# Kernel optimization log

Hardware: AMD Instinct MI355X
Metric: run time of the kernel (lower is better)

## Reference

```python
import jax, jax.numpy as jnp
import numpy as np
import math

B, S, D, H = 2, 2048, 512, 8
DK = D // H  # 64
NEG_INF = float('-inf')


def setup_inputs() -> dict:
    key = jax.random.key(0)
    ks = jax.random.split(key, 16)
    s = 1.0 / math.sqrt(D)
    return {
        'in_Q': jax.random.normal(ks[0], (B, S, D), jnp.float32),
        'in_K': jax.random.normal(ks[1], (B, S, D), jnp.float32),
        'in_V': jax.random.normal(ks[2], (B, S, D), jnp.float32),
        'row_pad_mask': jax.random.randint(ks[3], (B, S), 0, 2, jnp.int32),
        'col_pad_mask': jax.random.randint(ks[4], (B, S), 0, 2, jnp.int32),
        'W_Q': jax.random.uniform(ks[5], (D, D), jnp.float32, -s, s),
        'b_Q': jax.random.uniform(ks[6], (D,), jnp.float32, -s, s),
        'W_K': jax.random.uniform(ks[7], (D, D), jnp.float32, -s, s),
        'b_K': jax.random.uniform(ks[8], (D,), jnp.float32, -s, s),
        'W_V': jax.random.uniform(ks[9], (D, D), jnp.float32, -s, s),
        'b_V': jax.random.uniform(ks[10], (D,), jnp.float32, -s, s),
        'W_O': jax.random.uniform(ks[11], (D, D), jnp.float32, -s, s),
        'b_O': jax.random.uniform(ks[12], (D,), jnp.float32, -s, s),
    }


def reference(in_Q, in_K, in_V, row_pad_mask, col_pad_mask,
              W_Q, b_Q, W_K, b_K, W_V, b_V, W_O, b_O):
    b, sq, _ = in_Q.shape
    sk = in_K.shape[1]
    # projections (torch Linear: x @ W.T + b)
    Q = in_Q @ W_Q.T + b_Q
    K = in_K @ W_K.T + b_K
    V = in_V @ W_V.T + b_V
    # chunk along feature dim + stack == reshape to heads: [b, h, s, dk]
    Qh = Q.reshape(b, sq, H, DK).transpose(0, 2, 1, 3)
    Kh = K.reshape(b, sk, H, DK).transpose(0, 2, 1, 3)
    Vh = V.reshape(b, sk, H, DK).transpose(0, 2, 1, 3)
    scores = jnp.einsum('bhqd,bhkd->bhqk', Qh, Kh) / math.sqrt(DK)
    # causal mask (additive -inf above diagonal, as in the original)
    causal = jnp.triu(jnp.full((sq, sk), NEG_INF, scores.dtype), k=1)
    scores = scores + causal
    # padding masks: pad masks encode lengths via their row sums
    row_len = row_pad_mask.sum(axis=1)  # [b]
    col_len = col_pad_mask.sum(axis=1)
    row_np = jnp.arange(sq)[None, :] < row_len[:, None]  # [b, sq]
    col_np = jnp.arange(sk)[None, :] < col_len[:, None]  # [b, sk]
    non_pad = (row_np[:, :, None] & col_np[:, None, :])[:, None]  # [b,1,sq,sk]
    scores = jnp.where(non_pad, scores, NEG_INF)
    p = jax.nn.softmax(scores, axis=-1)
    p = jnp.nan_to_num(p)  # fully-masked rows -> 0 (matches torch nan_to_num)
    attn = jnp.einsum('bhqk,bhkd->bhqd', p, Vh)
    Hcat = attn.transpose(0, 2, 1, 3).reshape(b, sq, D)
    return Hcat @ W_O.T + b_O
```

## Files before the change

### kernel.cpp

```cpp
#include <hip/hip_runtime.h>

#define S_LEN 2048
#define D_MODEL 512
#define NHEAD 8
#define BATCH 2

typedef __attribute__((ext_vector_type(8))) short bf16x8;
typedef __attribute__((ext_vector_type(4))) float f32x4;

__device__ __forceinline__ unsigned short f2bf(float f) {
    union { float f; unsigned u; } v; v.f = f;
    unsigned u = v.u + 0x7FFFu + ((v.u >> 16) & 1u);
    return (unsigned short)(u >> 16);
}

__device__ __forceinline__ float ex2(float x) {
    return __builtin_amdgcn_exp2f(x);
}

__device__ __forceinline__ unsigned cvtpk(float lo, float hi) {
    unsigned r;
    asm("v_cvt_pk_bf16_f32 %0, %1, %2" : "=v"(r) : "v"(lo), "v"(hi));
    return r;
}

__device__ __forceinline__ void gl_lds16(const unsigned short* g, unsigned short* l) {
    __builtin_amdgcn_global_load_lds(
        (const __attribute__((address_space(1))) void*)g,
        (__attribute__((address_space(3))) void*)l,
        16, 0, 0);
}

__global__ __launch_bounds__(256) void cvtlens_kernel(
    const float* __restrict__ inQ, const float* __restrict__ inK, const float* __restrict__ inV,
    const float* __restrict__ WQ, const float* __restrict__ WK,
    const float* __restrict__ WV, const float* __restrict__ WO,
    const int* __restrict__ rpm, const int* __restrict__ cpm,
    unsigned short* __restrict__ Xbf, unsigned short* __restrict__ Wbf,
    int* __restrict__ lens)
{
    const int t = threadIdx.x;
    if (blockIdx.x < 2) {
        __shared__ int red[256];
        const int b = blockIdx.x;
        int sr = 0, sc2 = 0;
        for (int i = t; i < S_LEN; i += 256) {
            sr  += rpm[b * S_LEN + i];
            sc2 += cpm[b * S_LEN + i];
        }
        red[t] = sr;
        __syncthreads();
        for (int off = 128; off > 0; off >>= 1) {
            if (t < off) red[t] += red[t + off];
            __syncthreads();
        }
        if (t == 0) lens[b * 2 + 0] = red[0];
        __syncthreads();
        red[t] = sc2;
        __syncthreads();
        for (int off = 128; off > 0; off >>= 1) {
            if (t < off) red[t] += red[t + off];
            __syncthreads();
        }
        if (t == 0) lens[b * 2 + 1] = red[0];
    }

    const int NXC = 786432;
    const int NTOT = 917504;
    const int stride = gridDim.x * 256;
    for (int c = blockIdx.x * 256 + t; c < NTOT; c += stride) {
        if (c < NXC) {
            const int flat = c << 3;
            const int z = flat >> 21;
            const int off = flat & 2097151;
            const float* src = ((z == 0) ? inQ : (z == 1) ? inK : inV) + off;
            float4 a = *(const float4*)src;
            float4 d = *(const float4*)(src + 4);
            unsigned short* w = Xbf + flat;
            w[0] = f2bf(a.x); w[1] = f2bf(a.y); w[2] = f2bf(a.z); w[3] = f2bf(a.w);
            w[4] = f2bf(d.x); w[5] = f2bf(d.y); w[6] = f2bf(d.z); w[7] = f2bf(d.w);
        } else {
            const int wflat = (c - NXC) << 3;
            const int wz = wflat >> 18;
            const int off = wflat & 262143;
            const float* src = ((wz == 0) ? WQ : (wz == 1) ? WK : (wz == 2) ? WV : WO) + off;
            float4 a = *(const float4*)src;
            float4 d = *(const float4*)(src + 4);
            unsigned short* w = Wbf + wflat;
            w[0] = f2bf(a.x); w[1] = f2bf(a.y); w[2] = f2bf(a.z); w[3] = f2bf(a.w);
            w[4] = f2bf(d.x); w[5] = f2bf(d.y); w[6] = f2bf(d.z); w[7] = f2bf(d.w);
        }
    }
}

__global__ __launch_bounds__(256) void proj_gemm(
    const unsigned short* __restrict__ Xbf, const unsigned short* __restrict__ Wbf,
    const float* __restrict__ bQ, const float* __restrict__ bK, const float* __restrict__ bV,
    const int* __restrict__ lens,
    unsigned short* __restrict__ Qg, unsigned short* __restrict__ Kg,
    unsigned short* __restrict__ VTg)
{
    __shared__ __align__(16) unsigned short Xld[2][8192];
    __shared__ __align__(16) unsigned short Wld[2][8192];

    const int z = blockIdx.z;
    const int tileS = blockIdx.x * 128;
    const int tileF = blockIdx.y * 128;
    const int bb0 = tileS >> 11;
    const int rl = lens[bb0 * 2], cl = lens[bb0 * 2 + 1];
    const int limit = (z == 0) ? rl : cl;
    if ((tileS & 2047) >= limit) return;

    const unsigned short* X = Xbf + (size_t)z * (4096 * 512);
    const unsigned short* W = Wbf + (size_t)z * (512 * 512);
    const float* bias = (z == 0) ? bQ : (z == 1) ? bK : bV;

    const int t = threadIdx.x;
    const int wv = t >> 6, lane = t & 63, l15 = lane & 15, quad = lane >> 4;
    const int ro = lane >> 3;
    const int lc8 = ((lane & 7) ^ ro) * 8;

    const unsigned short* gX = X + (size_t)(tileS + wv * 32 + ro) * 512 + lc8;
    const unsigned short* gW = W + (size_t)(tileF + wv * 32 + ro) * 512 + lc8;
    const int wvo = wv * 2048;

    const int f_off = (wv & 1) * 64, s_off = (wv >> 1) * 64;
    const int swk = l15 & 7;

    f32x4 acc[4][4] = {};

    #pragma unroll
    for (int j = 0; j < 4; ++j) {
        gl_lds16(gX + j * 4096, &Xld[0][wvo + j * 512]);
        gl_lds16(gW + j * 4096, &Wld[0][wvo + j * 512]);
    }

    for (int kk = 0; kk < 8; ++kk) {
        __syncthreads();
        if (kk < 7) {
            const int k0 = (kk + 1) * 64;
            const int nb = (kk + 1) & 1;
            #pragma unroll
            for (int j = 0; j < 4; ++j) {
                gl_lds16(gX + k0 + j * 4096, &Xld[nb][wvo + j * 512]);
                gl_lds16(gW + k0 + j * 4096, &Wld[nb][wvo + j * 512]);
            }
        }
        const unsigned short* Xb = Xld[kk & 1];
        const unsigned short* Wb = Wld[kk & 1];
        #pragma unroll
        for (int kk2 = 0; kk2 < 2; ++kk2) {
            bf16x8 wf[4], xf[4];
            #pragma unroll
            for (int i = 0; i < 4; ++i) {
                const int rw = f_off + i * 16 + l15;
                wf[i] = *(const bf16x8*)(Wb + rw * 64 + ((kk2 * 4 + quad) ^ swk) * 8);
                const int rx = s_off + i * 16 + l15;
                xf[i] = *(const bf16x8*)(Xb + rx * 64 + ((kk2 * 4 + quad) ^ swk) * 8);
            }
            #pragma unroll
            for (int ft = 0; ft < 4; ++ft)
                #pragma unroll
                for (int st = 0; st < 4; ++st)
                    acc[ft][st] = __builtin_amdgcn_mfma_f32_16x16x32_bf16(
                        wf[ft], xf[st], acc[ft][st], 0, 0, 0);
        }
    }

    const float oscale = (z == 0) ? 0.18033688011112042f : 1.0f;
    #pragma unroll
    for (int ft = 0; ft < 4; ++ft) {
        const int f = tileF + f_off + ft * 16 + quad * 4;
        const int h = f >> 6, dk = f & 63;
        const float b0 = bias[f], b1 = bias[f + 1], b2 = bias[f + 2], b3 = bias[f + 3];
        #pragma unroll
        for (int st = 0; st < 4; ++st) {
            const int s = tileS + s_off + st * 16 + l15;
            const int bb = s >> 11, seq = s & 2047;
            const f32x4 a = acc[ft][st];
            if (z <= 1) {
                unsigned short* dst = ((z == 0) ? Qg : Kg)
                    + ((size_t)((bb * 8 + h) * 2048 + seq)) * 64 + dk;
                ushort4 u;
                u.x = f2bf((a[0] + b0) * oscale); u.y = f2bf((a[1] + b1) * oscale);
                u.z = f2bf((a[2] + b2) * oscale); u.w = f2bf((a[3] + b3) * oscale);
                *(ushort4*)dst = u;
            } else {
                unsigned short* dst = VTg
                    + ((size_t)((bb * 8 + h) * 64 + dk)) * 2048 + seq;
                dst[0]    = f2bf(a[0] + b0);
                dst[2048] = f2bf(a[1] + b1);
                dst[4096] = f2bf(a[2] + b2);
                dst[6144] = f2bf(a[3] + b3);
            }
        }
    }
}

__global__ __launch_bounds__(256) void attn_kernel(
    const unsigned short* __restrict__ Qg, const unsigned short* __restrict__ Kg,
    const unsigned short* __restrict__ VTg, const int* __restrict__ lens,
    unsigned short* __restrict__ AO)
{
    __shared__ __align__(16) char smem[35840];
    unsigned short* stage = (unsigned short*)smem;
    float* Ml = (float*)(smem + 34816);
    float* Ll = Ml + 128;

    const int t = threadIdx.x;
    const int wv = t >> 6, lane = t & 63, l15 = lane & 15, quad = lane >> 4;
    const int bh = blockIdx.y;
    const int b = bh >> 3, h = bh & 7;
    const int q0 = blockIdx.x * 32;
    const int rl = lens[b * 2], cl = lens[b * 2 + 1];

    if (q0 >= rl) {
        const int row = t >> 4, cg = t & 15;
        ushort4 zz = {0, 0, 0, 0};
        #pragma unroll
        for (int rr = 0; rr < 2; ++rr)
            *(ushort4*)(AO + ((size_t)(b * 2048 + q0 + rr * 16 + row)) * 512
                        + h * 64 + cg * 4) = zz;
        return;
    }

    bf16x8 aq[2][2];
    #pragma unroll
    for (int qs = 0; qs < 2; ++qs) {
        const unsigned short* Qrow = Qg + ((size_t)(bh * 2048 + q0 + qs * 16 + l15)) * 64;
        aq[qs][0] = *(const bf16x8*)(Qrow + quad * 8);
        aq[qs][1] = *(const bf16x8*)(Qrow + 32 + quad * 8);
    }

    unsigned short* stw = stage + wv * 4096;

    const int sro = lane >> 3;
    const int c0 = (((lane & 7) ^ (sro & 3)) << 3);
    const int sk = l15 & 7;
    const int sv = (l15 & 3) | ((l15 & 8) >> 1);
    const int skq0 = ((quad ^ sk) << 3), skq1 = (((quad + 4) ^ sk) << 3);
    const int svq0 = ((quad ^ sv) << 3), svq1 = (((quad + 4) ^ sv) << 3);

    f32x4 oacc[2][4] = {};
    float m_[2], l_[2];
    #pragma unroll
    for (int qs = 0; qs < 2; ++qs) { m_[qs] = -__builtin_inff(); l_[qs] = 0.f; }

    const int q_end = q0 + 32;
    const int kv_max = (cl < q_end) ? cl : q_end;
    const int ntiles = (kv_max + 63) >> 6;

    for (int kt = wv; kt < ntiles; kt += 4) {
        const int kv0 = kt * 64;

        {
            const unsigned short* kgb = Kg + ((size_t)(bh * 2048 + kv0 + sro)) * 64;
            #pragma unroll
            for (int j = 0; j < 8; ++j)
                gl_lds16(kgb + j * 512 + (c0 ^ ((j & 1) << 5)), stw + j * 512);
        }
        __builtin_amdgcn_s_waitcnt(0x0070);

        f32x4 sc[2][4];
        __builtin_amdgcn_s_setprio(1);
        #pragma unroll
        for (int ct = 0; ct < 4; ++ct) {
            const int grow = ((l15 >> 2) << 3) + ((ct & 1) << 2) + (l15 & 3)
                           + ((ct >> 1) << 5);
            const unsigned short* krow = stw + grow * 64;
            const bf16x8 kf0 = *(const bf16x8*)(krow + skq0);
            const bf16x8 kf1 = *(const bf16x8*)(krow + skq1);
            #pragma unroll
            for (int qs = 0; qs < 2; ++qs) {
                f32x4 zz = {};
                zz = __builtin_amdgcn_mfma_f32_16x16x32_bf16(kf0, aq[qs][0], zz, 0, 0, 0);
                sc[qs][ct] = __builtin_amdgcn_mfma_f32_16x16x32_bf16(kf1, aq[qs][1], zz, 0, 0, 0);
            }
        }
        __builtin_amdgcn_s_setprio(0);
        __builtin_amdgcn_s_waitcnt(0x0070);

        {
            const unsigned short* vgb = VTg + ((size_t)(bh * 64 + sro)) * 2048 + kv0;
            #pragma unroll
            for (int j = 0; j < 8; ++j)
                gl_lds16(vgb + j * 16384 + (c0 ^ ((j & 1) << 5)), stw + j * 512);
        }

        const bool full = (kv0 + 64 <= q0) && (kv0 + 64 <= cl) && (q_end <= rl);

        union { bf16x8 v; unsigned u[4]; } P0[2], P1[2];
        #pragma unroll
        for (int qs = 0; qs < 2; ++qs) {
            const int qme = q0 + qs * 16 + l15;
            if (!full) {
                #pragma unroll
                for (int ct = 0; ct < 4; ++ct) {
                    const int kvb = kv0 + quad * 8 + ((ct & 1) << 2) + ((ct >> 1) << 5);
                    #pragma unroll
                    for (int r = 0; r < 4; ++r) {
                        const int kv = kvb + r;
                        const bool valid = (qme < rl) && (kv < cl) && (kv <= qme);
                        sc[qs][ct][r] = valid ? sc[qs][ct][r] : -__builtin_inff();
                    }
                }
            }

            float mx = -__builtin_inff();
            #pragma unroll
            for (int ct = 0; ct < 4; ++ct)
                mx = fmaxf(mx, fmaxf(fmaxf(sc[qs][ct][0], sc[qs][ct][1]),
                                     fmaxf(sc[qs][ct][2], sc[qs][ct][3])));
            mx = fmaxf(mx, __shfl_xor(mx, 16));
            mx = fmaxf(mx, __shfl_xor(mx, 32));

            const float mnew = fmaxf(m_[qs], mx);
            const float alpha = (m_[qs] == -__builtin_inff()) ? 0.f : ex2(m_[qs] - mnew);
            const float mden = (mnew == -__builtin_inff()) ? 0.f : mnew;

            float psum = 0.f;
            #pragma unroll
            for (int ct = 0; ct < 4; ++ct) {
                #pragma unroll
                for (int r = 0; r < 4; ++r)
                    sc[qs][ct][r] = ex2(sc[qs][ct][r] - mden);
                psum += (sc[qs][ct][0] + sc[qs][ct][1]) + (sc[qs][ct][2] + sc[qs][ct][3]);
            }
            psum += __shfl_xor(psum, 16);
            psum += __shfl_xor(psum, 32);
            l_[qs] = alpha * l_[qs] + psum;
            m_[qs] = mnew;

            const float ar0 = __shfl(alpha, quad * 4 + 0);
            const float ar1 = __shfl(alpha, quad * 4 + 1);
            const float ar2 = __shfl(alpha, quad * 4 + 2);
            const float ar3 = __shfl(alpha, quad * 4 + 3);
            #pragma unroll
            for (int ct = 0; ct < 4; ++ct) {
                oacc[qs][ct][0] *= ar0; oacc[qs][ct][1] *= ar1;
                oacc[qs][ct][2] *= ar2; oacc[qs][ct][3] *= ar3;
            }

            P0[qs].u[0] = cvtpk(sc[qs][0][0], sc[qs][0][1]);
            P0[qs].u[1] = cvtpk(sc[qs][0][2], sc[qs][0][3]);
            P0[qs].u[2] = cvtpk(sc[qs][1][0], sc[qs][1][1]);
            P0[qs].u[3] = cvtpk(sc[qs][1][2], sc[qs][1][3]);
            P1[qs].u[0] = cvtpk(sc[qs][2][0], sc[qs][2][1]);
            P1[qs].u[1] = cvtpk(sc[qs][2][2], sc[qs][2][3]);
            P1[qs].u[2] = cvtpk(sc[qs][3][0], sc[qs][3][1]);
            P1[qs].u[3] = cvtpk(sc[qs][3][2], sc[qs][3][3]);
        }

        __builtin_amdgcn_s_waitcnt(0x0070);
        __builtin_amdgcn_s_setprio(1);
        #pragma unroll
        for (int ct = 0; ct < 4; ++ct) {
            const unsigned short* vrow = stw + (ct * 16 + l15) * 64;
            const bf16x8 vf0 = *(const bf16x8*)(vrow + svq0);
            const bf16x8 vf1 = *(const bf16x8*)(vrow + svq1);
            #pragma unroll
            for (int qs = 0; qs < 2; ++qs) {
                oacc[qs][ct] = __builtin_amdgcn_mfma_f32_16x16x32_bf16(P0[qs].v, vf0, oacc[qs][ct], 0, 0, 0);
                oacc[qs][ct] = __builtin_amdgcn_mfma_f32_16x16x32_bf16(P1[qs].v, vf1, oacc[qs][ct], 0, 0, 0);
            }
        }
        __builtin_amdgcn_s_setprio(0);
    }

    if (lane < 16) {
        #pragma unroll
        for (int qs = 0; qs < 2; ++qs) {
            Ml[wv * 32 + qs * 16 + l15] = m_[qs];
            Ll[wv * 32 + qs * 16 + l15] = l_[qs];
        }
    }
    __syncthreads();

    float* Po = (float*)smem;
    #pragma unroll
    for (int qs = 0; qs < 2; ++qs)
        #pragma unroll
        for (int ct = 0; ct < 4; ++ct)
            #pragma unroll
            for (int r = 0; r < 4; ++r)
                Po[wv * 2176 + (qs * 16 + quad * 4 + r) * 68 + ct * 16 + l15] = oacc[qs][ct][r];
    __syncthreads();

    const int row = t >> 4, cg = t & 15;
    #pragma unroll
    for (int rr = 0; rr < 2; ++rr) {
        const int orow = rr * 16 + row;
        float mw[4];
        float mstar = -__builtin_inff();
        #pragma unroll
        for (int w = 0; w < 4; ++w) {
            mw[w] = Ml[w * 32 + orow];
            mstar = fmaxf(mstar, mw[w]);
        }
        f32x4 o = {};
        if (mstar != -__builtin_inff()) {
            float lst = 0.f;
            #pragma unroll
            for (int w = 0; w < 4; ++w) {
                const float sw = (mw[w] == -__builtin_inff()) ? 0.f : ex2(mw[w] - mstar);
                lst += sw * Ll[w * 32 + orow];
                const f32x4 pv = *(const f32x4*)&Po[w * 2176 + orow * 68 + cg * 4];
                o[0] += sw * pv[0]; o[1] += sw * pv[1];
                o[2] += sw * pv[2]; o[3] += sw * pv[3];
            }
            const float inv = (lst > 0.f) ? 1.f / lst : 0.f;
            o[0] *= inv; o[1] *= inv; o[2] *= inv; o[3] *= inv;
        }
        ushort4 u;
        u.x = f2bf(o[0]); u.y = f2bf(o[1]); u.z = f2bf(o[2]); u.w = f2bf(o[3]);
        *(ushort4*)(AO + ((size_t)(b * 2048 + q0 + orow)) * 512 + h * 64 + cg * 4) = u;
    }
}

__global__ __launch_bounds__(256) void out_gemm(
    const unsigned short* __restrict__ AO, const unsigned short* __restrict__ Wbf,
    const float* __restrict__ bO, const int* __restrict__ lens, float* __restrict__ out)
{
    __shared__ __align__(16) unsigned short Xld[2][8192];
    __shared__ __align__(16) unsigned short Wld[2][8192];

    const int tileS = blockIdx.x * 128;
    const int tileF = blockIdx.y * 128;
    const int bb0 = tileS >> 11;
    const int rl = lens[bb0 * 2];
    const int t = threadIdx.x;

    if ((tileS & 2047) >= rl) {
        const int r0 = t >> 2;
        const int cg = (t & 3) * 32;
        float4 bv[8];
        #pragma unroll
        for (int j = 0; j < 8; ++j) bv[j] = *(const float4*)(bO + tileF + cg + j * 4);
        #pragma unroll
        for (int i = 0; i < 2; ++i) {
            float* orow = out + (size_t)(tileS + i * 64 + r0) * 512 + tileF + cg;
            #pragma unroll
            for (int j = 0; j < 8; ++j) *(float4*)(orow + j * 4) = bv[j];
        }
        return;
    }

    const unsigned short* W = Wbf + (size_t)3 * (512 * 512);
    const int wv = t >> 6, lane = t & 63, l15 = lane & 15, quad = lane >> 4;
    const int ro = lane >> 3;
    const int lc8 = ((lane & 7) ^ ro) * 8;

    const unsigned short* gX = AO + (size_t)(tileS + wv * 32 + ro) * 512 + lc8;
    const unsigned short* gW = W + (size_t)(tileF + wv * 32 + ro) * 512 + lc8;
    const int wvo = wv * 2048;

    const int f_off = (wv & 1) * 64, s_off = (wv >> 1) * 64;
    const int swk = l15 & 7;

    f32x4 acc[4][4] = {};

    #pragma unroll
    for (int j = 0; j < 4; ++j) {
        gl_lds16(gX + j * 4096, &Xld[0][wvo + j * 512]);
        gl_lds16(gW + j * 4096, &Wld[0][wvo + j * 512]);
    }

    for (int kk = 0; kk < 8; ++kk) {
        __syncthreads();
        if (kk < 7) {
            const int k0 = (kk + 1) * 64;
            const int nb = (kk + 1) & 1;
            #pragma unroll
            for (int j = 0; j < 4; ++j) {
                gl_lds16(gX + k0 + j * 4096, &Xld[nb][wvo + j * 512]);
                gl_lds16(gW + k0 + j * 4096, &Wld[nb][wvo + j * 512]);
            }
        }
        const unsigned short* Xb = Xld[kk & 1];
        const unsigned short* Wb = Wld[kk & 1];
        #pragma unroll
        for (int kk2 = 0; kk2 < 2; ++kk2) {
            bf16x8 wf[4], xf[4];
            #pragma unroll
            for (int i = 0; i < 4; ++i) {
                const int rw = f_off + i * 16 + l15;
                wf[i] = *(const bf16x8*)(Wb + rw * 64 + ((kk2 * 4 + quad) ^ swk) * 8);
                const int rx = s_off + i * 16 + l15;
                xf[i] = *(const bf16x8*)(Xb + rx * 64 + ((kk2 * 4 + quad) ^ swk) * 8);
            }
            #pragma unroll
            for (int ft = 0; ft < 4; ++ft)
                #pragma unroll
                for (int st = 0; st < 4; ++st)
                    acc[ft][st] = __builtin_amdgcn_mfma_f32_16x16x32_bf16(
                        wf[ft], xf[st], acc[ft][st], 0, 0, 0);
        }
    }

    #pragma unroll
    for (int ft = 0; ft < 4; ++ft) {
        const int f = tileF + f_off + ft * 16 + quad * 4;
        const float4 bv = *(const float4*)(bO + f);
        #pragma unroll
        for (int st = 0; st < 4; ++st) {
            const int s = tileS + s_off + st * 16 + l15;
            float4 o;
            o.x = acc[ft][st][0] + bv.x;
            o.y = acc[ft][st][1] + bv.y;
            o.z = acc[ft][st][2] + bv.z;
            o.w = acc[ft][st][3] + bv.w;
            *(float4*)(out + (size_t)s * 512 + f) = o;
        }
    }
}

extern "C" void kernel_launch(void* const* d_in, const int* in_sizes, int n_in,
                              void* d_out, int out_size, void* d_ws, size_t ws_size,
                              hipStream_t stream)
{
    const float* inQ = (const float*)d_in[0];
    const float* inK = (const float*)d_in[1];
    const float* inV = (const float*)d_in[2];
    const int*   rpm = (const int*)d_in[3];
    const int*   cpm = (const int*)d_in[4];
    const float* WQ  = (const float*)d_in[5];
    const float* bQ  = (const float*)d_in[6];
    const float* WK  = (const float*)d_in[7];
    const float* bK  = (const float*)d_in[8];
    const float* WV  = (const float*)d_in[9];
    const float* bV  = (const float*)d_in[10];
    const float* WO  = (const float*)d_in[11];
    const float* bO  = (const float*)d_in[12];
    float* out = (float*)d_out;

    char* ws = (char*)d_ws;
    unsigned short* Xbf = (unsigned short*)(ws);
    unsigned short* Wbf = (unsigned short*)(ws + 12582912);
    unsigned short* Qg  = (unsigned short*)(ws + 14680064);
    unsigned short* Kg  = (unsigned short*)(ws + 18874368);
    unsigned short* VTg = (unsigned short*)(ws + 23068672);
    unsigned short* AO  = (unsigned short*)(ws + 27262976);
    int* lens           = (int*)(ws + 31457280);

    cvtlens_kernel<<<dim3(1792), dim3(256), 0, stream>>>(
        inQ, inK, inV, WQ, WK, WV, WO, rpm, cpm, Xbf, Wbf, lens);
    proj_gemm<<<dim3(32, 4, 3), dim3(256), 0, stream>>>(
        Xbf, Wbf, bQ, bK, bV, lens, Qg, Kg, VTg);
    attn_kernel<<<dim3(64, 16), dim3(256), 0, stream>>>(Qg, Kg, VTg, lens, AO);
    out_gemm<<<dim3(32, 4), dim3(256), 0, stream>>>(AO, Wbf, bO, lens, out);
}
```

Before: 141.3 us.

## Fuse fp32-to-bf16 activation conversion into projection GEMM tile loads

The separate pass that converted the Q/K/V activations to bf16 in a workspace is removed. The projection GEMM now reads fp32 inputs directly into registers, converts them with packed cvt instructions, and stores them to LDS after the MFMA work of each k-step, keeping the double-buffer prefetch. This avoids a full write and re-read of 12MB of bf16 activations and shrinks the pre-pass to weights only. In exchange the GEMM does twice the global read bytes for X, holds more registers, and loses the async global-to-LDS path for X.

```diff
diff --git a/kernel.cpp b/kernel.cpp
--- a/kernel.cpp
+++ b/kernel.cpp
@@ -32,12 +32,10 @@
 }
 
 __global__ __launch_bounds__(256) void cvtlens_kernel(
-    const float* __restrict__ inQ, const float* __restrict__ inK, const float* __restrict__ inV,
     const float* __restrict__ WQ, const float* __restrict__ WK,
     const float* __restrict__ WV, const float* __restrict__ WO,
     const int* __restrict__ rpm, const int* __restrict__ cpm,
-    unsigned short* __restrict__ Xbf, unsigned short* __restrict__ Wbf,
-    int* __restrict__ lens)
+    unsigned short* __restrict__ Wbf, int* __restrict__ lens)
 {
     const int t = threadIdx.x;
     if (blockIdx.x < 2) {
@@ -65,36 +63,24 @@
         if (t == 0) lens[b * 2 + 1] = red[0];
     }
 
-    const int NXC = 786432;
-    const int NTOT = 917504;
+    const int NW = 131072;
     const int stride = gridDim.x * 256;
-    for (int c = blockIdx.x * 256 + t; c < NTOT; c += stride) {
-        if (c < NXC) {
-            const int flat = c << 3;
-            const int z = flat >> 21;
-            const int off = flat & 2097151;
-            const float* src = ((z == 0) ? inQ : (z == 1) ? inK : inV) + off;
-            float4 a = *(const float4*)src;
-            float4 d = *(const float4*)(src + 4);
-            unsigned short* w = Xbf + flat;
-            w[0] = f2bf(a.x); w[1] = f2bf(a.y); w[2] = f2bf(a.z); w[3] = f2bf(a.w);
-            w[4] = f2bf(d.x); w[5] = f2bf(d.y); w[6] = f2bf(d.z); w[7] = f2bf(d.w);
-        } else {
-            const int wflat = (c - NXC) << 3;
-            const int wz = wflat >> 18;
-            const int off = wflat & 262143;
-            const float* src = ((wz == 0) ? WQ : (wz == 1) ? WK : (wz == 2) ? WV : WO) + off;
-            float4 a = *(const float4*)src;
-            float4 d = *(const float4*)(src + 4);
-            unsigned short* w = Wbf + wflat;
-            w[0] = f2bf(a.x); w[1] = f2bf(a.y); w[2] = f2bf(a.z); w[3] = f2bf(a.w);
-            w[4] = f2bf(d.x); w[5] = f2bf(d.y); w[6] = f2bf(d.z); w[7] = f2bf(d.w);
-        }
+    for (int c = blockIdx.x * 256 + t; c < NW; c += stride) {
+        const int wflat = c << 3;
+        const int wz = wflat >> 18;
+        const int off = wflat & 262143;
+        const float* src = ((wz == 0) ? WQ : (wz == 1) ? WK : (wz == 2) ? WV : WO) + off;
+        float4 a = *(const float4*)src;
+        float4 d = *(const float4*)(src + 4);
+        unsigned short* w = Wbf + wflat;
+        w[0] = f2bf(a.x); w[1] = f2bf(a.y); w[2] = f2bf(a.z); w[3] = f2bf(a.w);
+        w[4] = f2bf(d.x); w[5] = f2bf(d.y); w[6] = f2bf(d.z); w[7] = f2bf(d.w);
     }
 }
 
 __global__ __launch_bounds__(256) void proj_gemm(
-    const unsigned short* __restrict__ Xbf, const unsigned short* __restrict__ Wbf,
+    const float* __restrict__ inQ, const float* __restrict__ inK,
+    const float* __restrict__ inV, const unsigned short* __restrict__ Wbf,
     const float* __restrict__ bQ, const float* __restrict__ bK, const float* __restrict__ bV,
     const int* __restrict__ lens,
     unsigned short* __restrict__ Qg, unsigned short* __restrict__ Kg,
@@ -111,7 +97,7 @@
     const int limit = (z == 0) ? rl : cl;
     if ((tileS & 2047) >= limit) return;
 
-    const unsigned short* X = Xbf + (size_t)z * (4096 * 512);
+    const float* Xs = (z == 0) ? inQ : (z == 1) ? inK : inV;
     const unsigned short* W = Wbf + (size_t)z * (512 * 512);
     const float* bias = (z == 0) ? bQ : (z == 1) ? bK : bV;
 
@@ -120,9 +106,10 @@
     const int ro = lane >> 3;
     const int lc8 = ((lane & 7) ^ ro) * 8;
 
-    const unsigned short* gX = X + (size_t)(tileS + wv * 32 + ro) * 512 + lc8;
+    const float* gXf = Xs + (size_t)(tileS + wv * 32 + ro) * 512 + lc8;
     const unsigned short* gW = W + (size_t)(tileF + wv * 32 + ro) * 512 + lc8;
     const int wvo = wv * 2048;
+    const int xdst = wvo + lane * 8;
 
     const int f_off = (wv & 1) * 64, s_off = (wv >> 1) * 64;
     const int swk = l15 & 7;
@@ -131,19 +118,27 @@
 
     #pragma unroll
     for (int j = 0; j < 4; ++j) {
-        gl_lds16(gX + j * 4096, &Xld[0][wvo + j * 512]);
+        const float* s = gXf + j * 4096;
+        float4 a = *(const float4*)s;
+        float4 d = *(const float4*)(s + 4);
+        uint4 u;
+        u.x = cvtpk(a.x, a.y); u.y = cvtpk(a.z, a.w);
+        u.z = cvtpk(d.x, d.y); u.w = cvtpk(d.z, d.w);
+        *(uint4*)&Xld[0][xdst + j * 512] = u;
         gl_lds16(gW + j * 4096, &Wld[0][wvo + j * 512]);
     }
 
     for (int kk = 0; kk < 8; ++kk) {
         __syncthreads();
+        float4 xa[4], xd[4];
         if (kk < 7) {
             const int k0 = (kk + 1) * 64;
-            const int nb = (kk + 1) & 1;
             #pragma unroll
             for (int j = 0; j < 4; ++j) {
-                gl_lds16(gX + k0 + j * 4096, &Xld[nb][wvo + j * 512]);
-                gl_lds16(gW + k0 + j * 4096, &Wld[nb][wvo + j * 512]);
+                const float* s = gXf + k0 + j * 4096;
+                xa[j] = *(const float4*)s;
+                xd[j] = *(const float4*)(s + 4);
+                gl_lds16(gW + k0 + j * 4096, &Wld[(kk + 1) & 1][wvo + j * 512]);
             }
         }
         const unsigned short* Xb = Xld[kk & 1];
@@ -164,6 +159,16 @@
                 for (int st = 0; st < 4; ++st)
                     acc[ft][st] = __builtin_amdgcn_mfma_f32_16x16x32_bf16(
                         wf[ft], xf[st], acc[ft][st], 0, 0, 0);
+        }
+        if (kk < 7) {
+            const int nb = (kk + 1) & 1;
+            #pragma unroll
+            for (int j = 0; j < 4; ++j) {
+                uint4 u;
+                u.x = cvtpk(xa[j].x, xa[j].y); u.y = cvtpk(xa[j].z, xa[j].w);
+                u.z = cvtpk(xd[j].x, xd[j].y); u.w = cvtpk(xd[j].z, xd[j].w);
+                *(uint4*)&Xld[nb][xdst + j * 512] = u;
+            }
         }
     }
 
@@ -534,7 +539,6 @@
     float* out = (float*)d_out;
 
     char* ws = (char*)d_ws;
-    unsigned short* Xbf = (unsigned short*)(ws);
     unsigned short* Wbf = (unsigned short*)(ws + 12582912);
     unsigned short* Qg  = (unsigned short*)(ws + 14680064);
     unsigned short* Kg  = (unsigned short*)(ws + 18874368);
@@ -542,10 +546,10 @@
     unsigned short* AO  = (unsigned short*)(ws + 27262976);
     int* lens           = (int*)(ws + 31457280);
 
-    cvtlens_kernel<<<dim3(1792), dim3(256), 0, stream>>>(
-        inQ, inK, inV, WQ, WK, WV, WO, rpm, cpm, Xbf, Wbf, lens);
+    cvtlens_kernel<<<dim3(512), dim3(256), 0, stream>>>(
+        WQ, WK, WV, WO, rpm, cpm, Wbf, lens);
     proj_gemm<<<dim3(32, 4, 3), dim3(256), 0, stream>>>(
-        Xbf, Wbf, bQ, bK, bV, lens, Qg, Kg, VTg);
+        inQ, inK, inV, Wbf, bQ, bK, bV, lens, Qg, Kg, VTg);
     attn_kernel<<<dim3(64, 16), dim3(256), 0, stream>>>(Qg, Kg, VTg, lens, AO);
     out_gemm<<<dim3(32, 4), dim3(256), 0, stream>>>(AO, Wbf, bO, lens, out);
 }
```

Result: no change. 141.5 us (+0.1%).
